# Kernel optimization log

Hardware: AMD Instinct MI355X
Metric: run time of the kernel (lower is better)

Reference implementation:

```python
import jax, jax.numpy as jnp
import numpy as np

DIM = 768
FF = 3072
E = 8          # num_experts
K = 2          # top_k
H = 12         # n_heads
HD = DIM // H  # head dim
LN_EPS = 1e-5


def _layernorm(x, g, b):
    m = jnp.mean(x, axis=-1, keepdims=True)
    v = jnp.var(x, axis=-1, keepdims=True)
    return (x - m) * jax.lax.rsqrt(v + LN_EPS) * g + b


def _attention(x, Wqkv, Wproj):
    B, T, D = x.shape
    qkv = (x @ Wqkv).reshape(B, T, 3, H, HD)
    q, k, v = qkv[:, :, 0], qkv[:, :, 1], qkv[:, :, 2]  # [B,T,H,HD]
    scores = jnp.einsum('bqhd,bkhd->bhqk', q, k) * jnp.float32(HD) ** -0.5
    attn = jax.nn.softmax(scores, axis=-1)  # non-causal SDPA
    out = jnp.einsum('bhqk,bkhd->bqhd', attn, v).reshape(B, T, D)
    return out @ Wproj


def _moe(x, Wrouter, W1, W2):
    # world_size == 1 path of MoEFeedForward.forward:
    # gate_and_sort -> per-expert FFN -> weighted index_add unpermute.
    # Equivalent math: out[t] = sum_k softmax(topk_logits)[t,k] * expert_{idx[t,k]}(x[t]).
    B, T, D = x.shape
    xf = x.reshape(-1, D)                       # [N, D]
    N = xf.shape[0]
    logits = xf @ Wrouter                        # [N, E]
    topk_w, topk_idx = jax.lax.top_k(logits, K)  # [N, K]
    topk_w = jax.nn.softmax(topk_w.astype(jnp.float32), axis=-1).astype(x.dtype)
    # Combined per-expert weight for each token (sums duplicates, 0 if unrouted).
    we = jnp.zeros((N, E), x.dtype).at[jnp.arange(N)[:, None], topk_idx].add(topk_w)  # [N, E]

    def body(acc, expert):
        W1e, W2e, we_e = expert                 # [D,FF], [FF,D], [N]
        h = jax.nn.gelu(xf @ W1e, approximate=False)  # exact GELU like nn.GELU()
        return acc + we_e[:, None] * (h @ W2e), None

    out, _ = jax.lax.scan(body, jnp.zeros_like(xf), (W1, W2, we.T))
    return out.reshape(B, T, D)


def setup_inputs() -> dict:
    key = jax.random.key(0)
    ks = jax.random.split(key, 7)
    B, T = 4, 1024
    init = lambda k, shape, fan: jax.random.normal(k, shape, jnp.float32) * (fan ** -0.5)
    return {
        'x': jax.random.normal(ks[0], (B, T, DIM), jnp.float32),
        'Wqkv': init(ks[1], (DIM, 3 * DIM), DIM),
        'Wproj': init(ks[2], (DIM, DIM), DIM),
        'Wrouter': init(ks[3], (DIM, E), DIM),
        'W1': init(ks[4], (E, DIM, FF), DIM),
        'W2': init(ks[5], (E, FF, DIM), FF),
        'ln1_g': jnp.ones((DIM,), jnp.float32), 'ln1_b': jnp.zeros((DIM,), jnp.float32),
        'ln2_g': jnp.ones((DIM,), jnp.float32), 'ln2_b': jnp.zeros((DIM,), jnp.float32),
    }


def reference(x, Wqkv, Wproj, Wrouter, W1, W2, ln1_g, ln1_b, ln2_g, ln2_b):
    # PipelinedMoEBlock: pre-LN attention + pre-LN MoE FFN, residual connections.
    x = x + _attention(_layernorm(x, ln1_g, ln1_b), Wqkv, Wproj)
    x = x + _moe(_layernorm(x, ln2_g, ln2_b), Wrouter, W1, W2)
    return x
```

## Files before the change

kernel.cpp:

```cpp
#include <hip/hip_runtime.h>
#include <math.h>

typedef unsigned short u16;
typedef __attribute__((ext_vector_type(8))) short short8;
typedef __attribute__((ext_vector_type(4))) float f32x4;

#define DIMC   768
#define TOK    4096
#define NQKVC  2304
#define FFC    3072
#define NEXP   8
#define NHEAD  12
#define HDIM   64
#define SEQ    1024
#define NBATCH 4
#define SLOTS  9216

__device__ __forceinline__ float bf2f(u16 v) {
    unsigned int u = ((unsigned int)v) << 16;
    float f; __builtin_memcpy(&f, &u, 4); return f;
}
__device__ __forceinline__ u16 f2bf(float f) {
    unsigned int u; __builtin_memcpy(&u, &f, 4);
    u = (u + 0x7fffu + ((u >> 16) & 1u)) >> 16;
    return (u16)u;
}

__device__ __forceinline__ void async16(u16* lds, const u16* gp) {
    __builtin_amdgcn_global_load_lds(
        (const __attribute__((address_space(1))) unsigned int*)gp,
        (__attribute__((address_space(3))) unsigned int*)lds, 16, 0, 0);
}

__global__ __launch_bounds__(256) void ln_split_kernel(const float* __restrict__ x,
                                                       const float* __restrict__ g,
                                                       const float* __restrict__ b,
                                                       u16* __restrict__ yh,
                                                       u16* __restrict__ yl) {
    int row = blockIdx.x, tid = threadIdx.x;
    const float* xr = x + (size_t)row * DIMC;
    float v[3];
#pragma unroll
    for (int i = 0; i < 3; i++) v[i] = xr[tid + 256 * i];
    float s = v[0] + v[1] + v[2];
    float q = v[0]*v[0] + v[1]*v[1] + v[2]*v[2];
#pragma unroll
    for (int o = 32; o; o >>= 1) { s += __shfl_down(s, o, 64); q += __shfl_down(q, o, 64); }
    __shared__ float rs[4], rq[4];
    if ((tid & 63) == 0) { rs[tid >> 6] = s; rq[tid >> 6] = q; }
    __syncthreads();
    s = rs[0] + rs[1] + rs[2] + rs[3];
    q = rq[0] + rq[1] + rq[2] + rq[3];
    float mean = s * (1.f / DIMC);
    float var  = q * (1.f / DIMC) - mean * mean;
    float rstd = rsqrtf(var + 1e-5f);
#pragma unroll
    for (int i = 0; i < 3; i++) {
        int c = tid + 256 * i;
        float o = (v[i] - mean) * rstd * g[c] + b[c];
        u16 h = f2bf(o);
        yh[(size_t)row * DIMC + c] = h;
        yl[(size_t)row * DIMC + c] = f2bf(o - bf2f(h));
    }
}

__global__ __launch_bounds__(256) void ln_bf_kernel(const float* __restrict__ x,
                                                    const float* __restrict__ g,
                                                    const float* __restrict__ b,
                                                    u16* __restrict__ yb,
                                                    float* __restrict__ yf) {
    int row = blockIdx.x, tid = threadIdx.x;
    const float* xr = x + (size_t)row * DIMC;
    float v[3];
#pragma unroll
    for (int i = 0; i < 3; i++) v[i] = xr[tid + 256 * i];
    float s = v[0] + v[1] + v[2];
    float q = v[0]*v[0] + v[1]*v[1] + v[2]*v[2];
#pragma unroll
    for (int o = 32; o; o >>= 1) { s += __shfl_down(s, o, 64); q += __shfl_down(q, o, 64); }
    __shared__ float rs[4], rq[4];
    if ((tid & 63) == 0) { rs[tid >> 6] = s; rq[tid >> 6] = q; }
    __syncthreads();
    s = rs[0] + rs[1] + rs[2] + rs[3];
    q = rq[0] + rq[1] + rq[2] + rq[3];
    float mean = s * (1.f / DIMC);
    float var  = q * (1.f / DIMC) - mean * mean;
    float rstd = rsqrtf(var + 1e-5f);
#pragma unroll
    for (int i = 0; i < 3; i++) {
        int c = tid + 256 * i;
        float o = (v[i] - mean) * rstd * g[c] + b[c];
        yb[(size_t)row * DIMC + c] = f2bf(o);
        yf[(size_t)row * DIMC + c] = o;
    }
}

__global__ __launch_bounds__(256) void transpose_split_kernel(
    const float* __restrict__ src, u16* __restrict__ dh, u16* __restrict__ dl,
    int s_rs, int d_rs, long s_bs, long d_bs) {
    __shared__ u16 th[32][33], tl[32][33];
    int z = blockIdx.z;
    const float* sb = src + (long)z * s_bs;
    int r0 = blockIdx.y * 32, c0 = blockIdx.x * 32;
    int tx = threadIdx.x & 31, ty = threadIdx.x >> 5;
#pragma unroll
    for (int i = 0; i < 4; i++) {
        float v = sb[(size_t)(r0 + ty + 8 * i) * s_rs + c0 + tx];
        u16 h = f2bf(v);
        th[ty + 8 * i][tx] = h;
        tl[ty + 8 * i][tx] = f2bf(v - bf2f(h));
    }
    __syncthreads();
#pragma unroll
    for (int i = 0; i < 4; i++) {
        size_t o = (long)z * d_bs + (size_t)(c0 + ty + 8 * i) * d_rs + r0 + tx;
        dh[o] = th[tx][ty + 8 * i];
        dl[o] = tl[tx][ty + 8 * i];
    }
}

__global__ __launch_bounds__(256) void transpose_f2b_kernel(
    const float* __restrict__ src, u16* __restrict__ dst,
    int s_rs, int d_rs, long s_bs, long d_bs) {
    __shared__ u16 tile[32][33];
    int z = blockIdx.z;
    const float* sb = src + (long)z * s_bs;
    int r0 = blockIdx.y * 32, c0 = blockIdx.x * 32;
    int tx = threadIdx.x & 31, ty = threadIdx.x >> 5;
#pragma unroll
    for (int i = 0; i < 4; i++)
        tile[ty + 8 * i][tx] = f2bf(sb[(size_t)(r0 + ty + 8 * i) * s_rs + c0 + tx]);
    __syncthreads();
#pragma unroll
    for (int i = 0; i < 4; i++)
        dst[(long)z * d_bs + (size_t)(c0 + ty + 8 * i) * d_rs + r0 + tx] = tile[tx][ty + 8 * i];
}

__global__ __launch_bounds__(256) void transpose_b2b_kernel(
    const u16* __restrict__ src, u16* __restrict__ dst,
    int s_rs, int d_rs, long s_bs1, int s_n1, long s_bs2, long d_bs) {
    __shared__ u16 tile[32][33];
    int z = blockIdx.z;
    const u16* sb = src + (long)(z / s_n1) * s_bs1 + (long)(z % s_n1) * s_bs2;
    u16* db = dst + (long)z * d_bs;
    int r0 = blockIdx.y * 32, c0 = blockIdx.x * 32;
    int tx = threadIdx.x & 31, ty = threadIdx.x >> 5;
#pragma unroll
    for (int i = 0; i < 4; i++)
        tile[ty + 8 * i][tx] = sb[(size_t)(r0 + ty + 8 * i) * s_rs + c0 + tx];
    __syncthreads();
#pragma unroll
    for (int i = 0; i < 4; i++)
        db[(size_t)(c0 + ty + 8 * i) * d_rs + r0 + tx] = tile[tx][ty + 8 * i];
}

template<int EPI, int OUT>
__global__ __launch_bounds__(256)
void gemm3_kernel(const u16* __restrict__ Ah, const u16* __restrict__ Al, int lda, long aBS,
                  const u16* __restrict__ Bh, const u16* __restrict__ Bl, int ldb, long bBS,
                  void* __restrict__ C0, void* __restrict__ C1, int ldc, long cBS,
                  int M, int N, int K, float alpha, const float* __restrict__ R) {
    __shared__ u16 Ash[128 * 32], Asl[128 * 32], Bsh[128 * 32], Bsl[128 * 32];
    int bm = blockIdx.y, bn = blockIdx.x, bz = blockIdx.z;
    int m0 = bm * 128, n0 = bn * 128;
    const u16* Ahb = Ah + (long)bz * aBS;
    const u16* Alb = Al + (long)bz * aBS;
    const u16* Bhb = Bh + (long)bz * bBS;
    const u16* Blb = Bl + (long)bz * bBS;
    int tid = threadIdx.x, wv = tid >> 6, ln = tid & 63;
    int quad = ln >> 4, l15 = ln & 15;
    int wm = wv & 1, wn = wv >> 1;
    f32x4 acc[4][4];
#pragma unroll
    for (int i = 0; i < 4; i++)
#pragma unroll
        for (int j = 0; j < 4; j++) acc[i][j] = (f32x4)0.f;
    int srow = ln >> 2, schk = (ln & 3) * 8;

    for (int k0 = 0; k0 < K; k0 += 32) {
#pragma unroll
        for (int j = 0; j < 2; j++) {
            int r = 32 * wv + 16 * j + srow;
            size_t ao = (size_t)(m0 + r) * lda + k0 + schk;
            async16(&Ash[(32 * wv + 16 * j) * 32], Ahb + ao);
            async16(&Asl[(32 * wv + 16 * j) * 32], Alb + ao);
            int gn = n0 + r; if (gn > N - 1) gn = N - 1;
            size_t bo = (size_t)gn * ldb + k0 + schk;
            async16(&Bsh[(32 * wv + 16 * j) * 32], Bhb + bo);
            async16(&Bsl[(32 * wv + 16 * j) * 32], Blb + bo);
        }
        __syncthreads();
        short8 ah[4], al4[4], bh[4], bl4[4];
#pragma unroll
        for (int mi = 0; mi < 4; mi++) {
            int off = (64 * wm + 16 * mi + l15) * 32 + quad * 8;
            ah[mi]  = *(const short8*)&Ash[off];
            al4[mi] = *(const short8*)&Asl[off];
        }
#pragma unroll
        for (int ni = 0; ni < 4; ni++) {
            int off = (64 * wn + 16 * ni + l15) * 32 + quad * 8;
            bh[ni]  = *(const short8*)&Bsh[off];
            bl4[ni] = *(const short8*)&Bsl[off];
        }
#pragma unroll
        for (int mi = 0; mi < 4; mi++)
#pragma unroll
            for (int ni = 0; ni < 4; ni++) {
                acc[mi][ni] = __builtin_amdgcn_mfma_f32_16x16x32_bf16(ah[mi],  bh[ni],  acc[mi][ni], 0, 0, 0);
                acc[mi][ni] = __builtin_amdgcn_mfma_f32_16x16x32_bf16(ah[mi],  bl4[ni], acc[mi][ni], 0, 0, 0);
                acc[mi][ni] = __builtin_amdgcn_mfma_f32_16x16x32_bf16(al4[mi], bh[ni],  acc[mi][ni], 0, 0, 0);
            }
        __syncthreads();
    }
#pragma unroll
    for (int mi = 0; mi < 4; mi++) {
#pragma unroll
        for (int r = 0; r < 4; r++) {
            int row = m0 + 64 * wm + 16 * mi + quad * 4 + r;
#pragma unroll
            for (int ni = 0; ni < 4; ni++) {
                int col = n0 + 64 * wn + 16 * ni + l15;
                if (col < N) {
                    size_t idx = (long)bz * cBS + (size_t)row * ldc + col;
                    float v = acc[mi][ni][r] * alpha;
                    if (EPI == 3) v += R[idx];
                    if (OUT == 1) ((float*)C0)[idx] = v;
                    else {
                        u16 h = f2bf(v);
                        ((u16*)C0)[idx] = h;
                        ((u16*)C1)[idx] = f2bf(v - bf2f(h));
                    }
                }
            }
        }
    }
}

template<int EPI, int OUTF>
__global__ __launch_bounds__(256)
void gemm_moe_kernel(const u16* __restrict__ A, int lda,
                     const u16* __restrict__ B, int ldb,
                     void* __restrict__ Cv, int ldc,
                     int N, int K,
                     const int* __restrict__ seg, long expStride) {
    __shared__ u16 As[128 * 32];
    __shared__ u16 Bs[128 * 32];
    int m0 = blockIdx.y * 128, n0 = blockIdx.x * 128;
    if (m0 >= seg[8]) return;
    int e = 0;
#pragma unroll
    for (int i = 1; i < 8; i++) if (m0 >= seg[i]) e = i;
    const u16* Bp = B + (long)e * expStride;
    int tid = threadIdx.x, wv = tid >> 6, ln = tid & 63;
    int quad = ln >> 4, l15 = ln & 15;
    int wm = wv & 1, wn = wv >> 1;
    f32x4 acc[4][4];
#pragma unroll
    for (int i = 0; i < 4; i++)
#pragma unroll
        for (int j = 0; j < 4; j++) acc[i][j] = (f32x4)0.f;
    int srow = ln >> 2, schk = (ln & 3) * 8;
    for (int k0 = 0; k0 < K; k0 += 32) {
#pragma unroll
        for (int j = 0; j < 2; j++) {
            int r = 32 * wv + 16 * j + srow;
            async16(&As[(32 * wv + 16 * j) * 32], A + (size_t)(m0 + r) * lda + k0 + schk);
            async16(&Bs[(32 * wv + 16 * j) * 32], Bp + (size_t)(n0 + r) * ldb + k0 + schk);
        }
        __syncthreads();
        short8 af[4], bfr[4];
#pragma unroll
        for (int mi = 0; mi < 4; mi++)
            af[mi] = *(const short8*)&As[(64 * wm + 16 * mi + l15) * 32 + quad * 8];
#pragma unroll
        for (int ni = 0; ni < 4; ni++)
            bfr[ni] = *(const short8*)&Bs[(64 * wn + 16 * ni + l15) * 32 + quad * 8];
#pragma unroll
        for (int mi = 0; mi < 4; mi++)
#pragma unroll
            for (int ni = 0; ni < 4; ni++)
                acc[mi][ni] = __builtin_amdgcn_mfma_f32_16x16x32_bf16(af[mi], bfr[ni], acc[mi][ni], 0, 0, 0);
        __syncthreads();
    }
#pragma unroll
    for (int mi = 0; mi < 4; mi++) {
#pragma unroll
        for (int r = 0; r < 4; r++) {
            int row = m0 + 64 * wm + 16 * mi + quad * 4 + r;
#pragma unroll
            for (int ni = 0; ni < 4; ni++) {
                int col = n0 + 64 * wn + 16 * ni + l15;
                float v = acc[mi][ni][r];
                if (EPI == 2) v = 0.5f * v * (1.f + erff(v * 0.70710678118654752f));
                size_t idx = (size_t)row * ldc + col;
                if (OUTF) ((float*)Cv)[idx] = v;
                else      ((u16*)Cv)[idx] = f2bf(v);
            }
        }
    }
}

__global__ __launch_bounds__(256) void softmax_split_kernel(float* __restrict__ S) {
    size_t row = blockIdx.x;
    float* p = S + row * (size_t)SEQ;
    u16* ph = (u16*)p;
    u16* pl = (u16*)p + SEQ;
    int tid = threadIdx.x;
    float v[4];
#pragma unroll
    for (int i = 0; i < 4; i++) v[i] = p[tid + 256 * i];
    float m = fmaxf(fmaxf(v[0], v[1]), fmaxf(v[2], v[3]));
#pragma unroll
    for (int o = 32; o; o >>= 1) m = fmaxf(m, __shfl_down(m, o, 64));
    __shared__ float red[4], red2[4];
    if ((tid & 63) == 0) red[tid >> 6] = m;
    __syncthreads();
    m = fmaxf(fmaxf(red[0], red[1]), fmaxf(red[2], red[3]));
    float e[4], s = 0.f;
#pragma unroll
    for (int i = 0; i < 4; i++) { e[i] = expf(v[i] - m); s += e[i]; }
#pragma unroll
    for (int o = 32; o; o >>= 1) s += __shfl_down(s, o, 64);
    if ((tid & 63) == 0) red2[tid >> 6] = s;
    __syncthreads();
    s = red2[0] + red2[1] + red2[2] + red2[3];
    float inv = 1.f / s;
#pragma unroll
    for (int i = 0; i < 4; i++) {
        int c = tid + 256 * i;
        float w = e[i] * inv;
        u16 h = f2bf(w);
        ph[c] = h;
        pl[c] = f2bf(w - bf2f(h));
    }
}

__global__ __launch_bounds__(256) void router_kernel(const float* __restrict__ h2f,
                                                     const float* __restrict__ Wr,
                                                     int* __restrict__ topk_idx,
                                                     float* __restrict__ topk_w,
                                                     int* __restrict__ counts) {
    int t = blockIdx.x, tid = threadIdx.x;
    __shared__ float part[256 * 8];
    float l[8];
#pragma unroll
    for (int e = 0; e < 8; e++) l[e] = 0.f;
    const float* xr = h2f + (size_t)t * DIMC;
#pragma unroll
    for (int i = 0; i < 3; i++) {
        int c = tid + 256 * i;
        float xv = xr[c];
        const float* wr = Wr + (size_t)c * NEXP;
#pragma unroll
        for (int e = 0; e < 8; e++) l[e] += xv * wr[e];
    }
#pragma unroll
    for (int e = 0; e < 8; e++) part[tid * 8 + e] = l[e];
    for (int s = 128; s; s >>= 1) {
        __syncthreads();
        if (tid < s)
#pragma unroll
            for (int e = 0; e < 8; e++) part[tid * 8 + e] += part[(tid + s) * 8 + e];
    }
    __syncthreads();
    if (tid == 0) {
        float lg[8];
#pragma unroll
        for (int e = 0; e < 8; e++) lg[e] = part[e];
        int i0 = 0;
        for (int e = 1; e < 8; e++) if (lg[e] > lg[i0]) i0 = e;
        int i1 = -1;
        for (int e = 0; e < 8; e++) if (e != i0 && (i1 < 0 || lg[e] > lg[i1])) i1 = e;
        float w1 = expf(lg[i1] - lg[i0]);
        float den = 1.f + w1;
        topk_idx[2 * t] = i0; topk_idx[2 * t + 1] = i1;
        topk_w[2 * t] = 1.f / den;  topk_w[2 * t + 1] = w1 / den;
        atomicAdd(&counts[i0], 1); atomicAdd(&counts[i1], 1);
    }
}

__global__ void offsets_kernel(const int* __restrict__ counts,
                               int* __restrict__ seg, int* __restrict__ cursor) {
    if (threadIdx.x == 0 && blockIdx.x == 0) {
        int off = 0;
        for (int e = 0; e < 8; e++) {
            seg[e] = off; cursor[e] = off;
            off += ((counts[e] + 127) / 128) * 128;
        }
        seg[8] = off;
    }
}

__global__ __launch_bounds__(256) void build_perm_kernel(
    const int* __restrict__ topk_idx, const float* __restrict__ topk_w,
    int* __restrict__ cursor, int* __restrict__ perm,
    float* __restrict__ gatew, int* __restrict__ slot_of) {
    int t = blockIdx.x * 256 + threadIdx.x;
    if (t >= TOK) return;
#pragma unroll
    for (int j = 0; j < 2; j++) {
        int e = topk_idx[2 * t + j];
        int slot = atomicAdd(&cursor[e], 1);
        perm[slot] = t;
        gatew[slot] = topk_w[2 * t + j];
        slot_of[2 * t + j] = slot;
    }
}

__global__ __launch_bounds__(192) void gather_kernel(const u16* __restrict__ h2,
                                                     const int* __restrict__ perm,
                                                     u16* __restrict__ xg) {
    int slot = blockIdx.x;
    int t = perm[slot];
    const uint2* s = (const uint2*)(h2 + (size_t)t * DIMC);
    uint2* d = (uint2*)(xg + (size_t)slot * DIMC);
    d[threadIdx.x] = s[threadIdx.x];
}

__global__ __launch_bounds__(192) void combine_kernel(
    const float* __restrict__ x1, const float* __restrict__ yg,
    const float* __restrict__ gatew, const int* __restrict__ slot_of,
    float* __restrict__ out) {
    int t = blockIdx.x;
    int s0 = slot_of[2 * t], s1 = slot_of[2 * t + 1];
    float w0 = gatew[s0], w1 = gatew[s1];
    int c = threadIdx.x * 4;
    const float* xr = x1 + (size_t)t * DIMC;
    const float* y0 = yg + (size_t)s0 * DIMC;
    const float* y1 = yg + (size_t)s1 * DIMC;
    float* orow = out + (size_t)t * DIMC;
#pragma unroll
    for (int k = 0; k < 4; k++)
        orow[c + k] = xr[c + k] + w0 * y0[c + k] + w1 * y1[c + k];
}

extern "C" void kernel_launch(void* const* d_in, const int* in_sizes, int n_in,
                              void* d_out, int out_size, void* d_ws, size_t ws_size,
                              hipStream_t stream) {
    const float* x       = (const float*)d_in[0];
    const float* Wqkv    = (const float*)d_in[1];
    const float* Wproj   = (const float*)d_in[2];
    const float* Wrouter = (const float*)d_in[3];
    const float* W1      = (const float*)d_in[4];
    const float* W2      = (const float*)d_in[5];
    const float* ln1g    = (const float*)d_in[6];
    const float* ln1b    = (const float*)d_in[7];
    const float* ln2g    = (const float*)d_in[8];
    const float* ln2b    = (const float*)d_in[9];
    float* out = (float*)d_out;
    char* ws = (char*)d_ws;

    const size_t o_x1   = 0;
    const size_t o_rout = 12582912;
    const size_t P      = 12845056;
    const size_t WS_REQ = 177995776;
    if (ws_size < WS_REQ) return;

    float* x1 = (float*)(ws + o_x1);
    float* Sc    = (float*)(ws + P);
    u16*   qkvh  = (u16*)(ws + P + 50331648);
    u16*   qkvl  = (u16*)(ws + P + 69206016);
    u16*   VTh   = (u16*)(ws + P + 88080384);
    u16*   VTl   = (u16*)(ws + P + 94371840);
    u16*   atth  = (u16*)(ws + P + 100663296);
    u16*   attl  = (u16*)(ws + P + 106954752);
    u16*   h1h   = (u16*)(ws + P + 113246208);
    u16*   h1l   = (u16*)(ws + P + 119537664);
    u16*   Wqh   = (u16*)(ws + P + 125829120);
    u16*   Wql   = (u16*)(ws + P + 129368064);
    u16*   Wph   = (u16*)(ws + P + 132907008);
    u16*   Wpl   = (u16*)(ws + P + 134086656);
    u16*   W1T   = (u16*)(ws + P);
    u16*   W2T   = (u16*)(ws + P + 37748736);
    u16*   h2    = (u16*)(ws + P + 75497472);
    float* h2f   = (float*)(ws + P + 81788928);
    u16*   xg    = (u16*)(ws + P + 94371840);
    u16*   hid   = (u16*)(ws + P + 108527616);
    float* yg    = (float*)(ws + P + 75497472);

    int*   counts   = (int*)(ws + o_rout + 0);
    int*   seg      = (int*)(ws + o_rout + 64);
    int*   cursor   = (int*)(ws + o_rout + 128);
    int*   topk_idx = (int*)(ws + o_rout + 1024);
    float* topk_w   = (float*)(ws + o_rout + 34816);
    int*   perm     = (int*)(ws + o_rout + 68608);
    float* gatew    = (float*)(ws + o_rout + 106496);
    int*   slot_of  = (int*)(ws + o_rout + 144384);

    const long EXPSTR = (long)DIMC * FFC;

    transpose_split_kernel<<<dim3(NQKVC/32, DIMC/32, 1), 256, 0, stream>>>(
        Wqkv, Wqh, Wql, NQKVC, DIMC, 0, 0);
    transpose_split_kernel<<<dim3(DIMC/32, DIMC/32, 1), 256, 0, stream>>>(
        Wproj, Wph, Wpl, DIMC, DIMC, 0, 0);
    ln_split_kernel<<<TOK, 256, 0, stream>>>(x, ln1g, ln1b, h1h, h1l);
    gemm3_kernel<0,2><<<dim3(NQKVC/128, TOK/128, 1), 256, 0, stream>>>(
        h1h, h1l, DIMC, 0, Wqh, Wql, DIMC, 0,
        qkvh, qkvl, NQKVC, 0, TOK, NQKVC, DIMC, 1.f, nullptr);
    transpose_b2b_kernel<<<dim3(HDIM/32, SEQ/32, NBATCH*NHEAD), 256, 0, stream>>>(
        qkvh + 2 * DIMC, VTh, NQKVC, SEQ, (long)SEQ * NQKVC, NHEAD, (long)HDIM, (long)HDIM * SEQ);
    transpose_b2b_kernel<<<dim3(HDIM/32, SEQ/32, NBATCH*NHEAD), 256, 0, stream>>>(
        qkvl + 2 * DIMC, VTl, NQKVC, SEQ, (long)SEQ * NQKVC, NHEAD, (long)HDIM, (long)HDIM * SEQ);
    for (int b = 0; b < NBATCH; b++) {
        const u16* qbh = qkvh + (size_t)b * SEQ * NQKVC;
        const u16* qbl = qkvl + (size_t)b * SEQ * NQKVC;
        gemm3_kernel<0,1><<<dim3(SEQ/128, SEQ/128, NHEAD), 256, 0, stream>>>(
            qbh, qbl, NQKVC, (long)HDIM,
            qbh + DIMC, qbl + DIMC, NQKVC, (long)HDIM,
            Sc, nullptr, SEQ, (long)SEQ * SEQ,
            SEQ, SEQ, HDIM, 0.125f, nullptr);
        softmax_split_kernel<<<NHEAD * SEQ, 256, 0, stream>>>(Sc);
        gemm3_kernel<0,2><<<dim3(1, SEQ/128, NHEAD), 256, 0, stream>>>(
            (const u16*)Sc, (const u16*)Sc + SEQ, 2 * SEQ, (long)SEQ * 2 * SEQ,
            VTh + (size_t)b * NHEAD * HDIM * SEQ, VTl + (size_t)b * NHEAD * HDIM * SEQ,
            SEQ, (long)HDIM * SEQ,
            atth + (size_t)b * SEQ * DIMC, attl + (size_t)b * SEQ * DIMC, DIMC, (long)HDIM,
            SEQ, HDIM, SEQ, 1.f, nullptr);
    }
    gemm3_kernel<3,1><<<dim3(DIMC/128, TOK/128, 1), 256, 0, stream>>>(
        atth, attl, DIMC, 0, Wph, Wpl, DIMC, 0,
        x1, nullptr, DIMC, 0, TOK, DIMC, DIMC, 1.f, x);

    transpose_f2b_kernel<<<dim3(FFC/32, DIMC/32, NEXP), 256, 0, stream>>>(
        W1, W1T, FFC, DIMC, EXPSTR, EXPSTR);
    transpose_f2b_kernel<<<dim3(DIMC/32, FFC/32, NEXP), 256, 0, stream>>>(
        W2, W2T, DIMC, FFC, EXPSTR, EXPSTR);
    ln_bf_kernel<<<TOK, 256, 0, stream>>>(x1, ln2g, ln2b, h2, h2f);
    (void)hipMemsetAsync(ws + o_rout, 0, 262144, stream);
    router_kernel<<<TOK, 256, 0, stream>>>(h2f, Wrouter, topk_idx, topk_w, counts);
    offsets_kernel<<<1, 64, 0, stream>>>(counts, seg, cursor);
    build_perm_kernel<<<16, 256, 0, stream>>>(topk_idx, topk_w, cursor, perm, gatew, slot_of);
    gather_kernel<<<SLOTS, 192, 0, stream>>>(h2, perm, xg);
    gemm_moe_kernel<2,0><<<dim3(FFC/128, SLOTS/128, 1), 256, 0, stream>>>(
        xg, DIMC, W1T, DIMC, hid, FFC, FFC, DIMC, seg, EXPSTR);
    gemm_moe_kernel<0,1><<<dim3(DIMC/128, SLOTS/128, 1), 256, 0, stream>>>(
        hid, FFC, W2T, FFC, yg, DIMC, DIMC, FFC, seg, EXPSTR);
    combine_kernel<<<TOK, 192, 0, stream>>>(x1, yg, gatew, slot_of, out);

    (void)in_sizes; (void)n_in; (void)out_size;
}
```

Before: 1.019 ms.

## Split-K the attention PV GEMM, narrow MoE down-proj tiles, use fast GELU

The attention P·V product was launched with a single N-tile per (128 query rows, head), which gave a small grid. It is replaced by a split-K kernel with 64-row tiles that accumulates into a zeroed fp32 buffer via atomics, followed by a separate hi/lo bf16 split pass. The MoE down-projection now uses a 64-wide N tile to double the number of blocks. Exact erff GELU is swapped for an Abramowitz-Stegun polynomial, and the N-bound clamps in gemm3 are removed. These changes add a memset, a split pass and atomic traffic, and the GELU approximation may add small error.

```diff
diff --git a/kernel.cpp b/kernel.cpp
--- a/kernel.cpp
+++ b/kernel.cpp
@@ -26,6 +26,16 @@
     return (u16)u;
 }
 
+__device__ __forceinline__ float fast_gelu(float v) {
+    float x = fabsf(v) * 0.70710678118654752f;
+    float t = __builtin_amdgcn_rcpf(1.f + 0.3275911f * x);
+    float y = t * (0.254829592f + t * (-0.284496736f + t * (1.421413741f +
+              t * (-1.453152027f + t * 1.061405429f))));
+    float er = 1.f - y * __expf(-x * x);
+    er = (v < 0.f) ? -er : er;
+    return 0.5f * v * (1.f + er);
+}
+
 __device__ __forceinline__ void async16(u16* lds, const u16* gp) {
     __builtin_amdgcn_global_load_lds(
         (const __attribute__((address_space(1))) unsigned int*)gp,
@@ -92,6 +102,19 @@
         float o = (v[i] - mean) * rstd * g[c] + b[c];
         yb[(size_t)row * DIMC + c] = f2bf(o);
         yf[(size_t)row * DIMC + c] = o;
+    }
+}
+
+__global__ __launch_bounds__(256) void split_hl_kernel(const float* __restrict__ src,
+                                                       u16* __restrict__ dh,
+                                                       u16* __restrict__ dl) {
+    size_t i = ((size_t)blockIdx.x * 256 + threadIdx.x) * 4;
+#pragma unroll
+    for (int k = 0; k < 4; k++) {
+        float v = src[i + k];
+        u16 h = f2bf(v);
+        dh[i + k] = h;
+        dl[i + k] = f2bf(v - bf2f(h));
     }
 }
 
@@ -184,8 +207,7 @@
             size_t ao = (size_t)(m0 + r) * lda + k0 + schk;
             async16(&Ash[(32 * wv + 16 * j) * 32], Ahb + ao);
             async16(&Asl[(32 * wv + 16 * j) * 32], Alb + ao);
-            int gn = n0 + r; if (gn > N - 1) gn = N - 1;
-            size_t bo = (size_t)gn * ldb + k0 + schk;
+            size_t bo = (size_t)(n0 + r) * ldb + k0 + schk;
             async16(&Bsh[(32 * wv + 16 * j) * 32], Bhb + bo);
             async16(&Bsl[(32 * wv + 16 * j) * 32], Blb + bo);
         }
@@ -221,20 +243,65 @@
 #pragma unroll
             for (int ni = 0; ni < 4; ni++) {
                 int col = n0 + 64 * wn + 16 * ni + l15;
-                if (col < N) {
-                    size_t idx = (long)bz * cBS + (size_t)row * ldc + col;
-                    float v = acc[mi][ni][r] * alpha;
-                    if (EPI == 3) v += R[idx];
-                    if (OUT == 1) ((float*)C0)[idx] = v;
-                    else {
-                        u16 h = f2bf(v);
-                        ((u16*)C0)[idx] = h;
-                        ((u16*)C1)[idx] = f2bf(v - bf2f(h));
-                    }
+                size_t idx = (long)bz * cBS + (size_t)row * ldc + col;
+                float v = acc[mi][ni][r] * alpha;
+                if (EPI == 3) v += R[idx];
+                if (OUT == 1) ((float*)C0)[idx] = v;
+                else {
+                    u16 h = f2bf(v);
+                    ((u16*)C0)[idx] = h;
+                    ((u16*)C1)[idx] = f2bf(v - bf2f(h));
                 }
             }
         }
     }
+}
+
+__global__ __launch_bounds__(256)
+void gemm3_pv_kernel(const u16* __restrict__ Ph,
+                     const u16* __restrict__ VTh_, const u16* __restrict__ VTl_,
+                     float* __restrict__ attf, int b) {
+    __shared__ u16 Ash[64 * 32], Asl[64 * 32], Bsh[64 * 32], Bsl[64 * 32];
+    int kz = blockIdx.x, qt = blockIdx.y, h = blockIdx.z;
+    int tid = threadIdx.x, wv = tid >> 6, ln = tid & 63;
+    int quad = ln >> 4, l15 = ln & 15;
+    const u16* Ah = Ph + (size_t)h * SEQ * 2 * SEQ;
+    const u16* Al = Ah + SEQ;
+    const u16* Bh = VTh_ + (size_t)h * HDIM * SEQ;
+    const u16* Bl = VTl_ + (size_t)h * HDIM * SEQ;
+    int m0 = qt * 64;
+    f32x4 acc[4];
+#pragma unroll
+    for (int i = 0; i < 4; i++) acc[i] = (f32x4)0.f;
+    int srow = ln >> 2, schk = (ln & 3) * 8;
+    int kbase = kz * (SEQ / 4);
+    for (int k0 = kbase; k0 < kbase + SEQ / 4; k0 += 32) {
+        int r = 16 * wv + srow;
+        async16(&Ash[(16 * wv) * 32], Ah + (size_t)(m0 + r) * 2 * SEQ + k0 + schk);
+        async16(&Asl[(16 * wv) * 32], Al + (size_t)(m0 + r) * 2 * SEQ + k0 + schk);
+        async16(&Bsh[(16 * wv) * 32], Bh + (size_t)r * SEQ + k0 + schk);
+        async16(&Bsl[(16 * wv) * 32], Bl + (size_t)r * SEQ + k0 + schk);
+        __syncthreads();
+        short8 a_h = *(const short8*)&Ash[(16 * wv + l15) * 32 + quad * 8];
+        short8 a_l = *(const short8*)&Asl[(16 * wv + l15) * 32 + quad * 8];
+#pragma unroll
+        for (int ni = 0; ni < 4; ni++) {
+            short8 b_h = *(const short8*)&Bsh[(16 * ni + l15) * 32 + quad * 8];
+            short8 b_l = *(const short8*)&Bsl[(16 * ni + l15) * 32 + quad * 8];
+            acc[ni] = __builtin_amdgcn_mfma_f32_16x16x32_bf16(a_h, b_h, acc[ni], 0, 0, 0);
+            acc[ni] = __builtin_amdgcn_mfma_f32_16x16x32_bf16(a_h, b_l, acc[ni], 0, 0, 0);
+            acc[ni] = __builtin_amdgcn_mfma_f32_16x16x32_bf16(a_l, b_h, acc[ni], 0, 0, 0);
+        }
+        __syncthreads();
+    }
+#pragma unroll
+    for (int ni = 0; ni < 4; ni++)
+#pragma unroll
+        for (int r = 0; r < 4; r++) {
+            int q = m0 + 16 * wv + quad * 4 + r;
+            int d = h * HDIM + 16 * ni + l15;
+            atomicAdd(&attf[((size_t)b * SEQ + q) * DIMC + d], acc[ni][r]);
+        }
 }
 
 template<int EPI, int OUTF>
@@ -292,13 +359,72 @@
             for (int ni = 0; ni < 4; ni++) {
                 int col = n0 + 64 * wn + 16 * ni + l15;
                 float v = acc[mi][ni][r];
-                if (EPI == 2) v = 0.5f * v * (1.f + erff(v * 0.70710678118654752f));
+                if (EPI == 2) v = fast_gelu(v);
                 size_t idx = (size_t)row * ldc + col;
                 if (OUTF) ((float*)Cv)[idx] = v;
                 else      ((u16*)Cv)[idx] = f2bf(v);
             }
         }
     }
+}
+
+__global__ __launch_bounds__(256)
+void gemm_moe_n64_kernel(const u16* __restrict__ A, int lda,
+                         const u16* __restrict__ B, int ldb,
+                         float* __restrict__ C, int ldc,
+                         int K, const int* __restrict__ seg, long expStride) {
+    __shared__ u16 As[128 * 32];
+    __shared__ u16 Bs[64 * 32];
+    int m0 = blockIdx.y * 128, n0 = blockIdx.x * 64;
+    if (m0 >= seg[8]) return;
+    int e = 0;
+#pragma unroll
+    for (int i = 1; i < 8; i++) if (m0 >= seg[i]) e = i;
+    const u16* Bp = B + (long)e * expStride;
+    int tid = threadIdx.x, wv = tid >> 6, ln = tid & 63;
+    int quad = ln >> 4, l15 = ln & 15;
+    f32x4 acc[2][4];
+#pragma unroll
+    for (int i = 0; i < 2; i++)
+#pragma unroll
+        for (int j = 0; j < 4; j++) acc[i][j] = (f32x4)0.f;
+    int srow = ln >> 2, schk = (ln & 3) * 8;
+    for (int k0 = 0; k0 < K; k0 += 32) {
+#pragma unroll
+        for (int j = 0; j < 2; j++) {
+            int r = 32 * wv + 16 * j + srow;
+            async16(&As[(32 * wv + 16 * j) * 32], A + (size_t)(m0 + r) * lda + k0 + schk);
+        }
+        {
+            int r = 16 * wv + srow;
+            async16(&Bs[(16 * wv) * 32], Bp + (size_t)(n0 + r) * ldb + k0 + schk);
+        }
+        __syncthreads();
+        short8 af[2], bfr[4];
+#pragma unroll
+        for (int mi = 0; mi < 2; mi++)
+            af[mi] = *(const short8*)&As[(32 * wv + 16 * mi + l15) * 32 + quad * 8];
+#pragma unroll
+        for (int ni = 0; ni < 4; ni++)
+            bfr[ni] = *(const short8*)&Bs[(16 * ni + l15) * 32 + quad * 8];
+#pragma unroll
+        for (int mi = 0; mi < 2; mi++)
+#pragma unroll
+            for (int ni = 0; ni < 4; ni++)
+                acc[mi][ni] = __builtin_amdgcn_mfma_f32_16x16x32_bf16(af[mi], bfr[ni], acc[mi][ni], 0, 0, 0);
+        __syncthreads();
+    }
+#pragma unroll
+    for (int mi = 0; mi < 2; mi++)
+#pragma unroll
+        for (int r = 0; r < 4; r++) {
+            int row = m0 + 32 * wv + 16 * mi + quad * 4 + r;
+#pragma unroll
+            for (int ni = 0; ni < 4; ni++) {
+                int col = n0 + 16 * ni + l15;
+                C[(size_t)row * ldc + col] = acc[mi][ni][r];
+            }
+        }
 }
 
 __global__ __launch_bounds__(256) void softmax_split_kernel(float* __restrict__ S) {
@@ -467,6 +593,7 @@
     u16*   attl  = (u16*)(ws + P + 106954752);
     u16*   h1h   = (u16*)(ws + P + 113246208);
     u16*   h1l   = (u16*)(ws + P + 119537664);
+    float* attf  = (float*)(ws + P + 113246208);
     u16*   Wqh   = (u16*)(ws + P + 125829120);
     u16*   Wql   = (u16*)(ws + P + 129368064);
     u16*   Wph   = (u16*)(ws + P + 132907008);
@@ -498,6 +625,7 @@
     gemm3_kernel<0,2><<<dim3(NQKVC/128, TOK/128, 1), 256, 0, stream>>>(
         h1h, h1l, DIMC, 0, Wqh, Wql, DIMC, 0,
         qkvh, qkvl, NQKVC, 0, TOK, NQKVC, DIMC, 1.f, nullptr);
+    (void)hipMemsetAsync(attf, 0, 12582912, stream);
     transpose_b2b_kernel<<<dim3(HDIM/32, SEQ/32, NBATCH*NHEAD), 256, 0, stream>>>(
         qkvh + 2 * DIMC, VTh, NQKVC, SEQ, (long)SEQ * NQKVC, NHEAD, (long)HDIM, (long)HDIM * SEQ);
     transpose_b2b_kernel<<<dim3(HDIM/32, SEQ/32, NBATCH*NHEAD), 256, 0, stream>>>(
@@ -511,13 +639,12 @@
             Sc, nullptr, SEQ, (long)SEQ * SEQ,
             SEQ, SEQ, HDIM, 0.125f, nullptr);
         softmax_split_kernel<<<NHEAD * SEQ, 256, 0, stream>>>(Sc);
-        gemm3_kernel<0,2><<<dim3(1, SEQ/128, NHEAD), 256, 0, stream>>>(
-            (const u16*)Sc, (const u16*)Sc + SEQ, 2 * SEQ, (long)SEQ * 2 * SEQ,
+        gemm3_pv_kernel<<<dim3(4, SEQ/64, NHEAD), 256, 0, stream>>>(
+            (const u16*)Sc,
             VTh + (size_t)b * NHEAD * HDIM * SEQ, VTl + (size_t)b * NHEAD * HDIM * SEQ,
-            SEQ, (long)HDIM * SEQ,
-            atth + (size_t)b * SEQ * DIMC, attl + (size_t)b * SEQ * DIMC, DIMC, (long)HDIM,
-            SEQ, HDIM, SEQ, 1.f, nullptr);
-    }
+            attf, b);
+    }
+    split_hl_kernel<<<(TOK * DIMC) / 1024, 256, 0, stream>>>(attf, atth, attl);
     gemm3_kernel<3,1><<<dim3(DIMC/128, TOK/128, 1), 256, 0, stream>>>(
         atth, attl, DIMC, 0, Wph, Wpl, DIMC, 0,
         x1, nullptr, DIMC, 0, TOK, DIMC, DIMC, 1.f, x);
@@ -534,8 +661,8 @@
     gather_kernel<<<SLOTS, 192, 0, stream>>>(h2, perm, xg);
     gemm_moe_kernel<2,0><<<dim3(FFC/128, SLOTS/128, 1), 256, 0, stream>>>(
         xg, DIMC, W1T, DIMC, hid, FFC, FFC, DIMC, seg, EXPSTR);
-    gemm_moe_kernel<0,1><<<dim3(DIMC/128, SLOTS/128, 1), 256, 0, stream>>>(
-        hid, FFC, W2T, FFC, yg, DIMC, DIMC, FFC, seg, EXPSTR);
+    gemm_moe_n64_kernel<<<dim3(DIMC/64, SLOTS/128, 1), 256, 0, stream>>>(
+        hid, FFC, W2T, FFC, yg, DIMC, FFC, seg, EXPSTR);
     combine_kernel<<<TOK, 192, 0, stream>>>(x1, yg, gatew, slot_of, out);
 
     (void)in_sizes; (void)n_in; (void)out_size;
```

Result: faster. 888.8 us (-12.7%).
